# Performance work log

Measured on AMD Instinct MI355X. Metric: run time of the kernel, lower is better.

Reference implementation:

```python
import jax, jax.numpy as jnp
import numpy as np

B, N, L, U = 128, 32, 100, 1024  # batch, n agents, traj length, hidden units


def setup_inputs() -> dict:
    key = jax.random.key(0)
    ks = jax.random.split(key, 16)
    s = 0.02
    return {
        "x": jax.random.normal(ks[0], (B, 4 * N, L), dtype=jnp.float32),
        "edges": jax.random.uniform(ks[1], (B, N, N), dtype=jnp.float32),
        # traj MLP: 4*L -> U -> U -> 1  (weights stored as [in, out])
        "traj1_w": s * jax.random.normal(ks[2], (4 * L, U), dtype=jnp.float32),
        "traj1_b": jnp.zeros((U,), dtype=jnp.float32),
        "traj2_w": s * jax.random.normal(ks[3], (U, U), dtype=jnp.float32),
        "traj2_b": jnp.zeros((U,), dtype=jnp.float32),
        "traj3_w": s * jax.random.normal(ks[4], (U, 1), dtype=jnp.float32),
        "traj3_b": jnp.zeros((1,), dtype=jnp.float32),
        # interaction MLP: 8*L -> U -> U -> 1
        "int1_w": s * jax.random.normal(ks[5], (8 * L, U), dtype=jnp.float32),
        "int1_b": jnp.zeros((U,), dtype=jnp.float32),
        "int2_w": s * jax.random.normal(ks[6], (U, U), dtype=jnp.float32),
        "int2_b": jnp.zeros((U,), dtype=jnp.float32),
        "int3_w": s * jax.random.normal(ks[7], (U, 1), dtype=jnp.float32),
        "int3_b": jnp.zeros((1,), dtype=jnp.float32),
    }


def _mlp3(h, w1, b1, w2, b2, w3, b3):
    h = jax.nn.relu(h @ w1 + b1)
    h = jax.nn.relu(h @ w2 + b2)
    return h @ w3 + b3


def reference(x, edges, traj1_w, traj1_b, traj2_w, traj2_b, traj3_w, traj3_b,
              int1_w, int1_b, int2_w, int2_b, int3_w, int3_b):
    b = x.shape[0]
    n = edges.shape[1]
    length = x.shape[2]
    x4 = x.reshape(b, n, 4, length)  # [B, n, 4, L]

    # per-trajectory energy: (B*n, 4*L) -> MLP -> (B, n) -> sum over agents
    te = _mlp3(x4.reshape(b * n, 4 * length),
               traj1_w, traj1_b, traj2_w, traj2_b, traj3_w, traj3_b)
    traj_e = te.reshape(b, n).sum(axis=1, keepdims=True)  # [B, 1]

    # pairwise interaction energy: concat sender/receiver channels -> (B*n*n, 8*L)
    xi = jnp.broadcast_to(x4[:, :, None], (b, n, n, 4, length))  # row index c1
    xj = jnp.broadcast_to(x4[:, None, :], (b, n, n, 4, length))  # col index c2
    pair = jnp.concatenate([xi, xj], axis=3).reshape(b * n * n, 8 * length)
    ie = _mlp3(pair, int1_w, int1_b, int2_w, int2_b, int3_w, int3_b)
    int_e = (edges * ie.reshape(b, n, n)).sum(axis=(1, 2))[:, None]  # [B, 1]

    return traj_e + int_e  # [B, 1]
```

## Files before the change

kernel.cpp:

```cpp
#include <hip/hip_runtime.h>

typedef unsigned short u16;
typedef unsigned int u32;
typedef short bf16x8_t __attribute__((ext_vector_type(8)));
typedef float f32x4_t __attribute__((ext_vector_type(4)));

#define OFF_XB   (0)
#define SZ_XB    (4096*416*2)
#define OFF_WCAT (OFF_XB + SZ_XB)
#define SZ_WCAT  (3072*416*2)
#define OFF_W2T  (OFF_WCAT + SZ_WCAT)
#define SZ_W2    (1024*1024*2)
#define OFF_W2I  (OFF_W2T + SZ_W2)
#define OFF_T1   (OFF_W2I + SZ_W2)
#define SZ_T1    (4096*1024*2)
#define OFF_P    (OFF_T1 + SZ_T1)
#define SZ_PQ    (4096*1024*4)
#define OFF_Q    (OFF_P + SZ_PQ)

__device__ __forceinline__ u16 f2bf(float f) {
  union { float f; u32 u; } v; v.f = f;
  u32 r = v.u + 0x7fffu + ((v.u >> 16) & 1u);
  return (u16)(r >> 16);
}
__device__ __forceinline__ u32 pk2(float a, float b) {
  u32 ua = __float_as_uint(fmaxf(a, 0.f)) + 0x8000u;
  u32 ub = __float_as_uint(fmaxf(b, 0.f)) + 0x8000u;
  return __builtin_amdgcn_perm(ub, ua, 0x07060302);
}
__device__ __forceinline__ void gload_lds16(const void* g, void* l) {
  __builtin_amdgcn_global_load_lds(
      (const __attribute__((address_space(1))) void*)g,
      (__attribute__((address_space(3))) void*)l, 16, 0, 0);
}

__device__ __forceinline__ void stage_sw(const u16* g, int ld, int row0, int k0,
                                         u16* lds, int nrow64, int wave, int lane) {
  int c = ((lane & 3) - ((lane >> 2) & 3)) & 3;
  const u16* src0 = g + (size_t)(row0 + (lane >> 2)) * ld + k0 + c * 8;
#pragma unroll
  for (int it = 0; it < nrow64; ++it) {
    int rbase = it * 64 + wave * 16;
    gload_lds16(src0 + (size_t)rbase * ld, lds + rbase * 32);
  }
}
__device__ __forceinline__ bf16x8_t read_sw(const u16* lds, int row, int quad) {
  int s = (quad + row) & 3;
  return *(const bf16x8_t*)(lds + row * 32 + s * 8);
}

__global__ void k_prep_x(const float* __restrict__ x, u16* __restrict__ Xb) {
  int k = blockIdx.x * 256 + threadIdx.x;
  int r = blockIdx.y;
  if (k < 416)
    Xb[(size_t)r * 416 + k] = (k < 400) ? f2bf(x[(size_t)r * 400 + k]) : (u16)0;
}

__global__ void k_prep_wcat(const float* __restrict__ t1w, const float* __restrict__ i1w,
                            u16* __restrict__ Wt) {
  int k = blockIdx.x * 256 + threadIdx.x;
  int n = blockIdx.y;
  if (k >= 416) return;
  float v = 0.f;
  if (k < 400) {
    if (n < 1024)      v = t1w[(size_t)k * 1024 + n];
    else if (n < 2048) v = i1w[(size_t)k * 1024 + (n - 1024)];
    else               v = i1w[(size_t)(400 + k) * 1024 + (n - 2048)];
  }
  Wt[(size_t)n * 416 + k] = f2bf(v);
}

__global__ void k_transpose(const float* __restrict__ W, u16* __restrict__ Wt) {
  __shared__ float t[32][33];
  int k0 = blockIdx.y * 32, n0 = blockIdx.x * 32;
  int tx = threadIdx.x, ty = threadIdx.y;
#pragma unroll
  for (int i = 0; i < 32; i += 8)
    t[ty + i][tx] = W[(size_t)(k0 + ty + i) * 1024 + n0 + tx];
  __syncthreads();
#pragma unroll
  for (int i = 0; i < 32; i += 8)
    Wt[(size_t)(n0 + ty + i) * 1024 + k0 + tx] = f2bf(t[tx][ty + i]);
}

__global__ __launch_bounds__(256) void k_gemm_l1(
    const u16* __restrict__ Xb, const u16* __restrict__ Wt,
    const float* __restrict__ b_t1, const float* __restrict__ b_i1,
    u16* __restrict__ T1, float* __restrict__ Pp, float* __restrict__ Qq) {
  __shared__ __align__(16) u16 al[128 * 32];
  __shared__ __align__(16) u16 bl[128 * 32];
  int tid = threadIdx.x, lane = tid & 63, wave = tid >> 6;
  int wr = wave & 1, wc = wave >> 1, ln = lane & 15, quad = lane >> 4;
  int m0 = blockIdx.x * 128, n0 = blockIdx.y * 128;
  f32x4_t acc[4][4];
#pragma unroll
  for (int i = 0; i < 4; ++i)
#pragma unroll
    for (int j = 0; j < 4; ++j) acc[i][j] = (f32x4_t){0.f, 0.f, 0.f, 0.f};

  for (int k0 = 0; k0 < 416; k0 += 32) {
    stage_sw(Xb, 416, m0, k0, al, 2, wave, lane);
    stage_sw(Wt, 416, n0, k0, bl, 2, wave, lane);
    __syncthreads();
    bf16x8_t af[4], bfr[4];
#pragma unroll
    for (int mt = 0; mt < 4; ++mt)
      af[mt] = read_sw(al, wr * 64 + mt * 16 + ln, quad);
#pragma unroll
    for (int nt = 0; nt < 4; ++nt)
      bfr[nt] = read_sw(bl, wc * 64 + nt * 16 + ln, quad);
#pragma unroll
    for (int mt = 0; mt < 4; ++mt)
#pragma unroll
      for (int nt = 0; nt < 4; ++nt)
        acc[mt][nt] = __builtin_amdgcn_mfma_f32_16x16x32_bf16(af[mt], bfr[nt], acc[mt][nt], 0, 0, 0);
    __syncthreads();
  }
  int seg = n0 >> 10;
#pragma unroll
  for (int nt = 0; nt < 4; ++nt) {
    int n_g = n0 + wc * 64 + nt * 16 + ln;
    int ns = n_g & 1023;
    float bias = (seg == 0) ? b_t1[ns] : (seg == 1 ? b_i1[ns] : 0.f);
#pragma unroll
    for (int mt = 0; mt < 4; ++mt) {
      f32x4_t c = acc[mt][nt];
#pragma unroll
      for (int r = 0; r < 4; ++r) {
        int m_g = m0 + wr * 64 + mt * 16 + quad * 4 + r;
        size_t idx = (size_t)m_g * 1024 + ns;
        float v = c[r] + bias;
        if (seg == 0)      T1[idx] = (u16)((__float_as_uint(fmaxf(v, 0.f)) + 0x8000u) >> 16);
        else if (seg == 1) Pp[idx] = v;
        else               Qq[idx] = v;
      }
    }
  }
}

__global__ __launch_bounds__(256) void k_traj23(
    const u16* __restrict__ T1, const u16* __restrict__ W2t,
    const float* __restrict__ b2, const float* __restrict__ w3,
    const float* __restrict__ b3, float* __restrict__ out) {
  __shared__ __align__(16) u16 al[128 * 32];
  __shared__ __align__(16) u16 bl[128 * 32];
  __shared__ float rowsum[128];
  int tid = threadIdx.x, lane = tid & 63, wave = tid >> 6;
  int wr = wave & 1, wc = wave >> 1, ln = lane & 15, quad = lane >> 4;
  int m0 = blockIdx.x * 128, n0 = blockIdx.y * 128;
  f32x4_t acc[4][4];
#pragma unroll
  for (int i = 0; i < 4; ++i)
#pragma unroll
    for (int j = 0; j < 4; ++j) acc[i][j] = (f32x4_t){0.f, 0.f, 0.f, 0.f};

  for (int k0 = 0; k0 < 1024; k0 += 32) {
    stage_sw(T1, 1024, m0, k0, al, 2, wave, lane);
    stage_sw(W2t, 1024, n0, k0, bl, 2, wave, lane);
    __syncthreads();
    bf16x8_t af[4], bfr[4];
#pragma unroll
    for (int mt = 0; mt < 4; ++mt)
      af[mt] = read_sw(al, wr * 64 + mt * 16 + ln, quad);
#pragma unroll
    for (int nt = 0; nt < 4; ++nt)
      bfr[nt] = read_sw(bl, wc * 64 + nt * 16 + ln, quad);
#pragma unroll
    for (int mt = 0; mt < 4; ++mt)
#pragma unroll
      for (int nt = 0; nt < 4; ++nt)
        acc[mt][nt] = __builtin_amdgcn_mfma_f32_16x16x32_bf16(af[mt], bfr[nt], acc[mt][nt], 0, 0, 0);
    __syncthreads();
  }
  float b2v[4], w3v[4];
#pragma unroll
  for (int nt = 0; nt < 4; ++nt) {
    int n = n0 + wc * 64 + nt * 16 + ln;
    b2v[nt] = b2[n]; w3v[nt] = w3[n];
  }
  if (tid < 128) rowsum[tid] = 0.f;
  __syncthreads();
#pragma unroll
  for (int mt = 0; mt < 4; ++mt) {
    float s[4] = {0.f, 0.f, 0.f, 0.f};
#pragma unroll
    for (int nt = 0; nt < 4; ++nt) {
      f32x4_t c = acc[mt][nt];
#pragma unroll
      for (int r = 0; r < 4; ++r) s[r] += fmaxf(c[r] + b2v[nt], 0.f) * w3v[nt];
    }
#pragma unroll
    for (int r = 0; r < 4; ++r) {
      for (int off = 1; off < 16; off <<= 1) s[r] += __shfl_xor(s[r], off);
      if (ln == 0) atomicAdd(&rowsum[wr * 64 + mt * 16 + quad * 4 + r], s[r]);
    }
  }
  __syncthreads();
  float contrib = 0.f;
  if (tid < 128) contrib = rowsum[tid] + (n0 == 0 ? b3[0] : 0.f);
  for (int off = 1; off < 32; off <<= 1) contrib += __shfl_xor(contrib, off);
  if ((lane & 31) == 0 && tid < 128) atomicAdd(&out[(m0 + tid) >> 5], contrib);
}

#define LDA_H 40
__global__ __launch_bounds__(256) void k_int_fused(
    const float* __restrict__ Pp, const float* __restrict__ Qq,
    const u16* __restrict__ W2t, const float* __restrict__ b2,
    const float* __restrict__ w3, const float* __restrict__ b3,
    const float* __restrict__ edges, float* __restrict__ out) {
  __shared__ __align__(16) u16 h1[64 * LDA_H];
  __shared__ __align__(16) u16 bl[256 * 32];
  __shared__ float rowsum[64];
  int tid = threadIdx.x, lane = tid & 63, wave = tid >> 6;
  int ln = lane & 15, quad = lane >> 4;
  int mtile = blockIdx.y;
  int n0 = blockIdx.x * 256;
  int b = mtile >> 4;
  int i0 = (mtile & 15) * 2;

  int rloc = tid >> 2;
  int kh = (tid & 3) * 8;
  const float* prow = Pp + ((size_t)(b * 32 + i0 + (rloc >> 5)) << 10) + kh;
  const float* qrow = Qq + ((size_t)(b * 32 + (rloc & 31)) << 10) + kh;

  f32x4_t acc[4][4];
#pragma unroll
  for (int i = 0; i < 4; ++i)
#pragma unroll
    for (int j = 0; j < 4; ++j) acc[i][j] = (f32x4_t){0.f, 0.f, 0.f, 0.f};

  for (int k0 = 0; k0 < 1024; k0 += 32) {
    const float4* pr = (const float4*)(prow + k0);
    const float4* qr = (const float4*)(qrow + k0);
    float4 p0 = pr[0], p1 = pr[1];
    float4 q0 = qr[0], q1 = qr[1];
    uint4 w;
    w.x = pk2(p0.x + q0.x, p0.y + q0.y);
    w.y = pk2(p0.z + q0.z, p0.w + q0.w);
    w.z = pk2(p1.x + q1.x, p1.y + q1.y);
    w.w = pk2(p1.z + q1.z, p1.w + q1.w);
    *(uint4*)(h1 + rloc * LDA_H + kh) = w;
    stage_sw(W2t, 1024, n0, k0, bl, 4, wave, lane);
    __syncthreads();
    bf16x8_t af[4], bfr[4];
#pragma unroll
    for (int mt = 0; mt < 4; ++mt)
      af[mt] = *(const bf16x8_t*)(h1 + (mt * 16 + ln) * LDA_H + quad * 8);
#pragma unroll
    for (int nt = 0; nt < 4; ++nt)
      bfr[nt] = read_sw(bl, wave * 64 + nt * 16 + ln, quad);
#pragma unroll
    for (int mt = 0; mt < 4; ++mt)
#pragma unroll
      for (int nt = 0; nt < 4; ++nt)
        acc[mt][nt] = __builtin_amdgcn_mfma_f32_16x16x32_bf16(af[mt], bfr[nt], acc[mt][nt], 0, 0, 0);
    __syncthreads();
  }
  float b2v[4], w3v[4];
#pragma unroll
  for (int nt = 0; nt < 4; ++nt) {
    int n = n0 + wave * 64 + nt * 16 + ln;
    b2v[nt] = b2[n]; w3v[nt] = w3[n];
  }
  if (tid < 64) rowsum[tid] = 0.f;
  __syncthreads();
#pragma unroll
  for (int mt = 0; mt < 4; ++mt) {
    float s[4] = {0.f, 0.f, 0.f, 0.f};
#pragma unroll
    for (int nt = 0; nt < 4; ++nt) {
      f32x4_t c = acc[mt][nt];
#pragma unroll
      for (int r = 0; r < 4; ++r) s[r] += fmaxf(c[r] + b2v[nt], 0.f) * w3v[nt];
    }
#pragma unroll
    for (int r = 0; r < 4; ++r) {
      for (int off = 1; off < 16; off <<= 1) s[r] += __shfl_xor(s[r], off);
      if (ln == 0) atomicAdd(&rowsum[mt * 16 + quad * 4 + r], s[r]);
    }
  }
  __syncthreads();
  if (wave == 0) {
    float ie = rowsum[lane] + (n0 == 0 ? b3[0] : 0.f);
    int i = i0 + (lane >> 5), j = lane & 31;
    float contrib = edges[(size_t)b * 1024 + i * 32 + j] * ie;
    for (int off = 1; off < 64; off <<= 1) contrib += __shfl_xor(contrib, off);
    if (lane == 0) atomicAdd(&out[b], contrib);
  }
}

extern "C" void kernel_launch(void* const* d_in, const int* in_sizes, int n_in,
                              void* d_out, int out_size, void* d_ws, size_t ws_size,
                              hipStream_t stream) {
  const float* x   = (const float*)d_in[0];
  const float* edges = (const float*)d_in[1];
  const float* t1w = (const float*)d_in[2];
  const float* t1b = (const float*)d_in[3];
  const float* t2w = (const float*)d_in[4];
  const float* t2b = (const float*)d_in[5];
  const float* t3w = (const float*)d_in[6];
  const float* t3b = (const float*)d_in[7];
  const float* i1w = (const float*)d_in[8];
  const float* i1b = (const float*)d_in[9];
  const float* i2w = (const float*)d_in[10];
  const float* i2b = (const float*)d_in[11];
  const float* i3w = (const float*)d_in[12];
  const float* i3b = (const float*)d_in[13];
  char* ws = (char*)d_ws;
  u16*   Xb   = (u16*)(ws + OFF_XB);
  u16*   Wcat = (u16*)(ws + OFF_WCAT);
  u16*   W2t  = (u16*)(ws + OFF_W2T);
  u16*   W2i  = (u16*)(ws + OFF_W2I);
  u16*   T1   = (u16*)(ws + OFF_T1);
  float* Pp   = (float*)(ws + OFF_P);
  float* Qq   = (float*)(ws + OFF_Q);
  float* out  = (float*)d_out;

  hipMemsetAsync(out, 0, 128 * sizeof(float), stream);
  k_prep_x<<<dim3(2, 4096), 256, 0, stream>>>(x, Xb);
  k_prep_wcat<<<dim3(2, 3072), 256, 0, stream>>>(t1w, i1w, Wcat);
  k_transpose<<<dim3(32, 32), dim3(32, 8), 0, stream>>>(t2w, W2t);
  k_transpose<<<dim3(32, 32), dim3(32, 8), 0, stream>>>(i2w, W2i);
  k_gemm_l1<<<dim3(32, 24), 256, 0, stream>>>(Xb, Wcat, t1b, i1b, T1, Pp, Qq);
  k_traj23<<<dim3(32, 8), 256, 0, stream>>>(T1, W2t, t2b, t3w, t3b, out);
  k_int_fused<<<dim3(4, 2048), 256, 0, stream>>>(Pp, Qq, W2i, i2b, i3w, i3b, edges, out);
}
```

Baseline: 584.0 us.

## Double-buffer LDS tiles and prefetch P/Q in fused interaction kernel

Turns the K loop of the fused interaction GEMM into a two-stage software pipeline. The h1 and W2 LDS tiles are double-buffered, and the next step's P/Q rows are loaded into registers while the current MFMAs run. One barrier per iteration is removed and global-load latency can overlap with matrix math. In exchange, LDS use per block doubles and register pressure rises, which may lower occupancy.

```diff
diff --git a/kernel.cpp b/kernel.cpp
--- a/kernel.cpp
+++ b/kernel.cpp
@@ -208,8 +208,8 @@
     const u16* __restrict__ W2t, const float* __restrict__ b2,
     const float* __restrict__ w3, const float* __restrict__ b3,
     const float* __restrict__ edges, float* __restrict__ out) {
-  __shared__ __align__(16) u16 h1[64 * LDA_H];
-  __shared__ __align__(16) u16 bl[256 * 32];
+  __shared__ __align__(16) u16 h1[2 * 64 * LDA_H];
+  __shared__ __align__(16) u16 bl[2 * 256 * 32];
   __shared__ float rowsum[64];
   int tid = threadIdx.x, lane = tid & 63, wave = tid >> 6;
   int ln = lane & 15, quad = lane >> 4;
@@ -229,33 +229,58 @@
 #pragma unroll
     for (int j = 0; j < 4; ++j) acc[i][j] = (f32x4_t){0.f, 0.f, 0.f, 0.f};
 
-  for (int k0 = 0; k0 < 1024; k0 += 32) {
-    const float4* pr = (const float4*)(prow + k0);
-    const float4* qr = (const float4*)(qrow + k0);
-    float4 p0 = pr[0], p1 = pr[1];
-    float4 q0 = qr[0], q1 = qr[1];
+  float4 p0, p1, q0, q1;
+  {
+    const float4* pr = (const float4*)(prow);
+    const float4* qr = (const float4*)(qrow);
+    p0 = pr[0]; p1 = pr[1]; q0 = qr[0]; q1 = qr[1];
     uint4 w;
     w.x = pk2(p0.x + q0.x, p0.y + q0.y);
     w.y = pk2(p0.z + q0.z, p0.w + q0.w);
     w.z = pk2(p1.x + q1.x, p1.y + q1.y);
     w.w = pk2(p1.z + q1.z, p1.w + q1.w);
     *(uint4*)(h1 + rloc * LDA_H + kh) = w;
-    stage_sw(W2t, 1024, n0, k0, bl, 4, wave, lane);
-    __syncthreads();
+    stage_sw(W2t, 1024, n0, 0, bl, 4, wave, lane);
+    const float4* prn = (const float4*)(prow + 32);
+    const float4* qrn = (const float4*)(qrow + 32);
+    p0 = prn[0]; p1 = prn[1]; q0 = qrn[0]; q1 = qrn[1];
+  }
+  __syncthreads();
+
+  for (int k0 = 0; k0 < 1024; k0 += 32) {
+    int cur = (k0 >> 5) & 1, nxt = cur ^ 1;
+    u16* h1c = h1 + cur * 64 * LDA_H;
+    u16* blc = bl + cur * 256 * 32;
     bf16x8_t af[4], bfr[4];
 #pragma unroll
     for (int mt = 0; mt < 4; ++mt)
-      af[mt] = *(const bf16x8_t*)(h1 + (mt * 16 + ln) * LDA_H + quad * 8);
+      af[mt] = *(const bf16x8_t*)(h1c + (mt * 16 + ln) * LDA_H + quad * 8);
 #pragma unroll
     for (int nt = 0; nt < 4; ++nt)
-      bfr[nt] = read_sw(bl, wave * 64 + nt * 16 + ln, quad);
+      bfr[nt] = read_sw(blc, wave * 64 + nt * 16 + ln, quad);
+    if (k0 + 32 < 1024)
+      stage_sw(W2t, 1024, n0, k0 + 32, bl + nxt * 256 * 32, 4, wave, lane);
 #pragma unroll
     for (int mt = 0; mt < 4; ++mt)
 #pragma unroll
       for (int nt = 0; nt < 4; ++nt)
         acc[mt][nt] = __builtin_amdgcn_mfma_f32_16x16x32_bf16(af[mt], bfr[nt], acc[mt][nt], 0, 0, 0);
-    __syncthreads();
-  }
+    if (k0 + 32 < 1024) {
+      uint4 w;
+      w.x = pk2(p0.x + q0.x, p0.y + q0.y);
+      w.y = pk2(p0.z + q0.z, p0.w + q0.w);
+      w.z = pk2(p1.x + q1.x, p1.y + q1.y);
+      w.w = pk2(p1.z + q1.z, p1.w + q1.w);
+      *(uint4*)(h1 + nxt * 64 * LDA_H + rloc * LDA_H + kh) = w;
+      if (k0 + 64 < 1024) {
+        const float4* prn = (const float4*)(prow + k0 + 64);
+        const float4* qrn = (const float4*)(qrow + k0 + 64);
+        p0 = prn[0]; p1 = prn[1]; q0 = qrn[0]; q1 = qrn[1];
+      }
+    }
+    __syncthreads();
+  }
+
   float b2v[4], w3v[4];
 #pragma unroll
   for (int nt = 0; nt < 4; ++nt) {
```

After: 547.0 us. 1.07x faster.

## Build interaction A-fragments in registers and double-buffer W2 staging

Applied to the files above, without the earlier changes.

The fused interaction layer-2 kernel now builds the relu(P_i+Q_j) bf16 A-fragments directly in registers from prefetched P/Q values, removing the LDS h1 staging and one barrier per k-step. The block tile changes from 64x256 to 128x128 with a 2x2 wave layout. The W2 tile is double-buffered so the next k-slice loads while MFMAs run, and launch bounds request 3 blocks per CU. The cost is more register pressure from prefetched float4s, and P/Q re-reads now happen per wave instead of once per block.

```diff
diff --git a/kernel.cpp b/kernel.cpp
--- a/kernel.cpp
+++ b/kernel.cpp
@@ -28,6 +28,14 @@
   u32 ub = __float_as_uint(fmaxf(b, 0.f)) + 0x8000u;
   return __builtin_amdgcn_perm(ub, ua, 0x07060302);
 }
+__device__ __forceinline__ bf16x8_t mk_frag(float4 pa, float4 pb, float4 qa, float4 qb) {
+  union { u32 w[4]; bf16x8_t v; } u;
+  u.w[0] = pk2(pa.x + qa.x, pa.y + qa.y);
+  u.w[1] = pk2(pa.z + qa.z, pa.w + qa.w);
+  u.w[2] = pk2(pb.x + qb.x, pb.y + qb.y);
+  u.w[3] = pk2(pb.z + qb.z, pb.w + qb.w);
+  return u.v;
+}
 __device__ __forceinline__ void gload_lds16(const void* g, void* l) {
   __builtin_amdgcn_global_load_lds(
       (const __attribute__((address_space(1))) void*)g,
@@ -202,26 +210,24 @@
   if ((lane & 31) == 0 && tid < 128) atomicAdd(&out[(m0 + tid) >> 5], contrib);
 }
 
-#define LDA_H 40
-__global__ __launch_bounds__(256) void k_int_fused(
+__global__ __launch_bounds__(256, 3) void k_int_fused(
     const float* __restrict__ Pp, const float* __restrict__ Qq,
     const u16* __restrict__ W2t, const float* __restrict__ b2,
     const float* __restrict__ w3, const float* __restrict__ b3,
     const float* __restrict__ edges, float* __restrict__ out) {
-  __shared__ __align__(16) u16 h1[64 * LDA_H];
-  __shared__ __align__(16) u16 bl[256 * 32];
-  __shared__ float rowsum[64];
+  __shared__ __align__(16) u16 bl[2 * 128 * 32];
+  __shared__ float rowsum[128];
   int tid = threadIdx.x, lane = tid & 63, wave = tid >> 6;
-  int ln = lane & 15, quad = lane >> 4;
+  int wr = wave & 1, wc = wave >> 1, ln = lane & 15, quad = lane >> 4;
   int mtile = blockIdx.y;
-  int n0 = blockIdx.x * 256;
-  int b = mtile >> 4;
-  int i0 = (mtile & 15) * 2;
-
-  int rloc = tid >> 2;
-  int kh = (tid & 3) * 8;
-  const float* prow = Pp + ((size_t)(b * 32 + i0 + (rloc >> 5)) << 10) + kh;
-  const float* qrow = Qq + ((size_t)(b * 32 + (rloc & 31)) << 10) + kh;
+  int n0 = blockIdx.x * 128;
+  int b = mtile >> 3;
+  int i0 = (mtile & 7) * 4;
+
+  const float* p0r = Pp + ((size_t)(b * 32 + i0 + 2 * wr) << 10) + quad * 8;
+  const float* p1r = p0r + 1024;
+  const float* q0r = Qq + ((size_t)(b * 32 + ln) << 10) + quad * 8;
+  const float* q1r = q0r + (16 << 10);
 
   f32x4_t acc[4][4];
 #pragma unroll
@@ -229,40 +235,49 @@
 #pragma unroll
     for (int j = 0; j < 4; ++j) acc[i][j] = (f32x4_t){0.f, 0.f, 0.f, 0.f};
 
+  float4 P0a = *(const float4*)(p0r),     P0b = *(const float4*)(p0r + 4);
+  float4 P1a = *(const float4*)(p1r),     P1b = *(const float4*)(p1r + 4);
+  float4 Q0a = *(const float4*)(q0r),     Q0b = *(const float4*)(q0r + 4);
+  float4 Q1a = *(const float4*)(q1r),     Q1b = *(const float4*)(q1r + 4);
+  stage_sw(W2t, 1024, n0, 0, bl, 2, wave, lane);
+  __syncthreads();
+
   for (int k0 = 0; k0 < 1024; k0 += 32) {
-    const float4* pr = (const float4*)(prow + k0);
-    const float4* qr = (const float4*)(qrow + k0);
-    float4 p0 = pr[0], p1 = pr[1];
-    float4 q0 = qr[0], q1 = qr[1];
-    uint4 w;
-    w.x = pk2(p0.x + q0.x, p0.y + q0.y);
-    w.y = pk2(p0.z + q0.z, p0.w + q0.w);
-    w.z = pk2(p1.x + q1.x, p1.y + q1.y);
-    w.w = pk2(p1.z + q1.z, p1.w + q1.w);
-    *(uint4*)(h1 + rloc * LDA_H + kh) = w;
-    stage_sw(W2t, 1024, n0, k0, bl, 4, wave, lane);
-    __syncthreads();
-    bf16x8_t af[4], bfr[4];
-#pragma unroll
-    for (int mt = 0; mt < 4; ++mt)
-      af[mt] = *(const bf16x8_t*)(h1 + (mt * 16 + ln) * LDA_H + quad * 8);
+    int cur = (k0 >> 5) & 1, nxt = cur ^ 1;
+    bf16x8_t af0 = mk_frag(P0a, P0b, Q0a, Q0b);
+    bf16x8_t af1 = mk_frag(P0a, P0b, Q1a, Q1b);
+    bf16x8_t af2 = mk_frag(P1a, P1b, Q0a, Q0b);
+    bf16x8_t af3 = mk_frag(P1a, P1b, Q1a, Q1b);
+    if (k0 + 32 < 1024) {
+      int kn = k0 + 32;
+      P0a = *(const float4*)(p0r + kn); P0b = *(const float4*)(p0r + kn + 4);
+      P1a = *(const float4*)(p1r + kn); P1b = *(const float4*)(p1r + kn + 4);
+      Q0a = *(const float4*)(q0r + kn); Q0b = *(const float4*)(q0r + kn + 4);
+      Q1a = *(const float4*)(q1r + kn); Q1b = *(const float4*)(q1r + kn + 4);
+      stage_sw(W2t, 1024, n0, kn, bl + nxt * 128 * 32, 2, wave, lane);
+    }
+    const u16* blc = bl + cur * 128 * 32;
+    bf16x8_t bfr[4];
 #pragma unroll
     for (int nt = 0; nt < 4; ++nt)
-      bfr[nt] = read_sw(bl, wave * 64 + nt * 16 + ln, quad);
-#pragma unroll
-    for (int mt = 0; mt < 4; ++mt)
-#pragma unroll
-      for (int nt = 0; nt < 4; ++nt)
-        acc[mt][nt] = __builtin_amdgcn_mfma_f32_16x16x32_bf16(af[mt], bfr[nt], acc[mt][nt], 0, 0, 0);
-    __syncthreads();
-  }
+      bfr[nt] = read_sw(blc, wc * 64 + nt * 16 + ln, quad);
+#pragma unroll
+    for (int nt = 0; nt < 4; ++nt) {
+      acc[0][nt] = __builtin_amdgcn_mfma_f32_16x16x32_bf16(af0, bfr[nt], acc[0][nt], 0, 0, 0);
+      acc[1][nt] = __builtin_amdgcn_mfma_f32_16x16x32_bf16(af1, bfr[nt], acc[1][nt], 0, 0, 0);
+      acc[2][nt] = __builtin_amdgcn_mfma_f32_16x16x32_bf16(af2, bfr[nt], acc[2][nt], 0, 0, 0);
+      acc[3][nt] = __builtin_amdgcn_mfma_f32_16x16x32_bf16(af3, bfr[nt], acc[3][nt], 0, 0, 0);
+    }
+    __syncthreads();
+  }
+
   float b2v[4], w3v[4];
 #pragma unroll
   for (int nt = 0; nt < 4; ++nt) {
-    int n = n0 + wave * 64 + nt * 16 + ln;
+    int n = n0 + wc * 64 + nt * 16 + ln;
     b2v[nt] = b2[n]; w3v[nt] = w3[n];
   }
-  if (tid < 64) rowsum[tid] = 0.f;
+  if (tid < 128) rowsum[tid] = 0.f;
   __syncthreads();
 #pragma unroll
   for (int mt = 0; mt < 4; ++mt) {
@@ -276,17 +291,18 @@
 #pragma unroll
     for (int r = 0; r < 4; ++r) {
       for (int off = 1; off < 16; off <<= 1) s[r] += __shfl_xor(s[r], off);
-      if (ln == 0) atomicAdd(&rowsum[mt * 16 + quad * 4 + r], s[r]);
-    }
-  }
-  __syncthreads();
-  if (wave == 0) {
-    float ie = rowsum[lane] + (n0 == 0 ? b3[0] : 0.f);
-    int i = i0 + (lane >> 5), j = lane & 31;
-    float contrib = edges[(size_t)b * 1024 + i * 32 + j] * ie;
-    for (int off = 1; off < 64; off <<= 1) contrib += __shfl_xor(contrib, off);
-    if (lane == 0) atomicAdd(&out[b], contrib);
-  }
+      if (ln == 0) atomicAdd(&rowsum[wr * 64 + mt * 16 + quad * 4 + r], s[r]);
+    }
+  }
+  __syncthreads();
+  float contrib = 0.f;
+  if (tid < 128) {
+    float ie = rowsum[tid] + (n0 == 0 ? b3[0] : 0.f);
+    int i = i0 + (tid >> 5), j = tid & 31;
+    contrib = edges[(size_t)b * 1024 + i * 32 + j] * ie;
+  }
+  for (int off = 1; off < 64; off <<= 1) contrib += __shfl_xor(contrib, off);
+  if (lane == 0 && wave < 2) atomicAdd(&out[b], contrib);
 }
 
 extern "C" void kernel_launch(void* const* d_in, const int* in_sizes, int n_in,
@@ -323,5 +339,5 @@
   k_transpose<<<dim3(32, 32), dim3(32, 8), 0, stream>>>(i2w, W2i);
   k_gemm_l1<<<dim3(32, 24), 256, 0, stream>>>(Xb, Wcat, t1b, i1b, T1, Pp, Qq);
   k_traj23<<<dim3(32, 8), 256, 0, stream>>>(T1, W2t, t2b, t3w, t3b, out);
-  k_int_fused<<<dim3(4, 2048), 256, 0, stream>>>(Pp, Qq, W2i, i2b, i3w, i3b, edges, out);
-}
+  k_int_fused<<<dim3(8, 1024), 256, 0, stream>>>(Pp, Qq, W2i, i2b, i3w, i3b, edges, out);
+}
```

After: 802.2 us. 37.4% more time.

## Double-buffer LDS tiles and prefetch P/Q registers in fused interaction GEMM

Applied to the files above, without the earlier changes.

Splits the h1 and weight LDS tiles into two buffers and software-pipelines the K loop. The next weight tile is staged and the next P/Q fragments are loaded into registers while MFMAs run on the current buffer, which halves the barriers per K step. This is meant to hide global-load latency behind matrix math, at the cost of twice the LDS and more live registers, which may reduce occupancy.

```diff
diff --git a/kernel.cpp b/kernel.cpp
--- a/kernel.cpp
+++ b/kernel.cpp
@@ -203,13 +203,23 @@
 }
 
 #define LDA_H 40
+__device__ __forceinline__ void pack_h1(u16* dst, int rloc, int kh,
+                                        float4 p0, float4 p1, float4 q0, float4 q1) {
+  uint4 w;
+  w.x = pk2(p0.x + q0.x, p0.y + q0.y);
+  w.y = pk2(p0.z + q0.z, p0.w + q0.w);
+  w.z = pk2(p1.x + q1.x, p1.y + q1.y);
+  w.w = pk2(p1.z + q1.z, p1.w + q1.w);
+  *(uint4*)(dst + rloc * LDA_H + kh) = w;
+}
+
 __global__ __launch_bounds__(256) void k_int_fused(
     const float* __restrict__ Pp, const float* __restrict__ Qq,
     const u16* __restrict__ W2t, const float* __restrict__ b2,
     const float* __restrict__ w3, const float* __restrict__ b3,
     const float* __restrict__ edges, float* __restrict__ out) {
-  __shared__ __align__(16) u16 h1[64 * LDA_H];
-  __shared__ __align__(16) u16 bl[256 * 32];
+  __shared__ __align__(16) u16 h1[2 * 64 * LDA_H];
+  __shared__ __align__(16) u16 bl[2 * 256 * 32];
   __shared__ float rowsum[64];
   int tid = threadIdx.x, lane = tid & 63, wave = tid >> 6;
   int ln = lane & 15, quad = lane >> 4;
@@ -229,33 +239,70 @@
 #pragma unroll
     for (int j = 0; j < 4; ++j) acc[i][j] = (f32x4_t){0.f, 0.f, 0.f, 0.f};
 
-  for (int k0 = 0; k0 < 1024; k0 += 32) {
-    const float4* pr = (const float4*)(prow + k0);
-    const float4* qr = (const float4*)(qrow + k0);
-    float4 p0 = pr[0], p1 = pr[1];
-    float4 q0 = qr[0], q1 = qr[1];
-    uint4 w;
-    w.x = pk2(p0.x + q0.x, p0.y + q0.y);
-    w.y = pk2(p0.z + q0.z, p0.w + q0.w);
-    w.z = pk2(p1.x + q1.x, p1.y + q1.y);
-    w.w = pk2(p1.z + q1.z, p1.w + q1.w);
-    *(uint4*)(h1 + rloc * LDA_H + kh) = w;
-    stage_sw(W2t, 1024, n0, k0, bl, 4, wave, lane);
-    __syncthreads();
-    bf16x8_t af[4], bfr[4];
-#pragma unroll
-    for (int mt = 0; mt < 4; ++mt)
-      af[mt] = *(const bf16x8_t*)(h1 + (mt * 16 + ln) * LDA_H + quad * 8);
-#pragma unroll
-    for (int nt = 0; nt < 4; ++nt)
-      bfr[nt] = read_sw(bl, wave * 64 + nt * 16 + ln, quad);
-#pragma unroll
-    for (int mt = 0; mt < 4; ++mt)
+  float4 pA0, pA1, qA0, qA1;
+  float4 pB0, pB1, qB0, qB1;
+
+  {
+    float4 t0 = *(const float4*)(prow),     t1 = *(const float4*)(prow + 4);
+    float4 u0 = *(const float4*)(qrow),     u1 = *(const float4*)(qrow + 4);
+    pack_h1(h1, rloc, kh, t0, t1, u0, u1);
+    stage_sw(W2t, 1024, n0, 0, bl, 4, wave, lane);
+    pA0 = *(const float4*)(prow + 32); pA1 = *(const float4*)(prow + 36);
+    qA0 = *(const float4*)(qrow + 32); qA1 = *(const float4*)(qrow + 36);
+  }
+  __syncthreads();
+
+  for (int kp = 0; kp < 1024; kp += 64) {
+    {
+      int k0 = kp;
+      if (k0 + 64 < 1024) {
+        pB0 = *(const float4*)(prow + k0 + 64); pB1 = *(const float4*)(prow + k0 + 68);
+        qB0 = *(const float4*)(qrow + k0 + 64); qB1 = *(const float4*)(qrow + k0 + 68);
+      }
+      if (k0 + 32 < 1024)
+        stage_sw(W2t, 1024, n0, k0 + 32, bl + 256 * 32, 4, wave, lane);
+      bf16x8_t af[4], bfr[4];
+#pragma unroll
+      for (int mt = 0; mt < 4; ++mt)
+        af[mt] = *(const bf16x8_t*)(h1 + (mt * 16 + ln) * LDA_H + quad * 8);
 #pragma unroll
       for (int nt = 0; nt < 4; ++nt)
-        acc[mt][nt] = __builtin_amdgcn_mfma_f32_16x16x32_bf16(af[mt], bfr[nt], acc[mt][nt], 0, 0, 0);
-    __syncthreads();
-  }
+        bfr[nt] = read_sw(bl, wave * 64 + nt * 16 + ln, quad);
+#pragma unroll
+      for (int mt = 0; mt < 4; ++mt)
+#pragma unroll
+        for (int nt = 0; nt < 4; ++nt)
+          acc[mt][nt] = __builtin_amdgcn_mfma_f32_16x16x32_bf16(af[mt], bfr[nt], acc[mt][nt], 0, 0, 0);
+      if (k0 + 32 < 1024)
+        pack_h1(h1 + 64 * LDA_H, rloc, kh, pA0, pA1, qA0, qA1);
+      __syncthreads();
+    }
+    {
+      int k0 = kp + 32;
+      if (k0 + 64 < 1024) {
+        pA0 = *(const float4*)(prow + k0 + 64); pA1 = *(const float4*)(prow + k0 + 68);
+        qA0 = *(const float4*)(qrow + k0 + 64); qA1 = *(const float4*)(qrow + k0 + 68);
+      }
+      if (k0 + 32 < 1024)
+        stage_sw(W2t, 1024, n0, k0 + 32, bl, 4, wave, lane);
+      bf16x8_t af[4], bfr[4];
+#pragma unroll
+      for (int mt = 0; mt < 4; ++mt)
+        af[mt] = *(const bf16x8_t*)(h1 + 64 * LDA_H + (mt * 16 + ln) * LDA_H + quad * 8);
+#pragma unroll
+      for (int nt = 0; nt < 4; ++nt)
+        bfr[nt] = read_sw(bl + 256 * 32, wave * 64 + nt * 16 + ln, quad);
+#pragma unroll
+      for (int mt = 0; mt < 4; ++mt)
+#pragma unroll
+        for (int nt = 0; nt < 4; ++nt)
+          acc[mt][nt] = __builtin_amdgcn_mfma_f32_16x16x32_bf16(af[mt], bfr[nt], acc[mt][nt], 0, 0, 0);
+      if (k0 + 32 < 1024)
+        pack_h1(h1, rloc, kh, pB0, pB1, qB0, qB1);
+      __syncthreads();
+    }
+  }
+
   float b2v[4], w3v[4];
 #pragma unroll
   for (int nt = 0; nt < 4; ++nt) {
```

Result: slower. 644.2 us (+10.3%).
